# Optimization experiments

Measured on AMD Instinct MI355X. Metric: run time of the kernel, lower is better.

Reference implementation:

```python
import jax, jax.numpy as jnp
import numpy as np

INV_SQRT_2 = 0.5 ** 0.5

B, N, D_IN, D_OUT = 2, 50000, 64, 64
E = 800000


def setup_inputs() -> dict:
    key = jax.random.key(0)
    k1, k2, k3, k4, k5, k6 = jax.random.split(key, 6)
    x = jax.random.normal(k1, (B, N, D_IN, 3), dtype=jnp.float32)
    W_node = jax.random.normal(k2, (D_OUT, D_IN), dtype=jnp.float32)
    W_edge = jax.random.normal(k3, (D_OUT, D_IN), dtype=jnp.float32)
    norm_coeff = jax.random.uniform(k4, (N,), dtype=jnp.float32)
    src = jax.random.randint(k5, (E,), 0, N, dtype=jnp.int32)
    dst = jax.random.randint(k6, (E,), 0, N, dtype=jnp.int32)
    return {"x": x, "W_node": W_node, "W_edge": W_edge,
            "norm_coeff": norm_coeff, "src": src, "dst": dst}


def reference(x, W_node, W_edge, norm_coeff, src, dst):
    # x: (B, N, D_IN, 3)
    y_node = jnp.einsum('oi,bnik->bnok', W_node, x)      # (B, N, D_OUT, 3)
    y_edge = jnp.einsum('oi,bnik->bnok', W_edge, x)      # (B, N, D_OUT, 3)
    # gather by src along node axis, scatter-add into dst
    gathered = y_edge[:, src]                            # (B, E, D_OUT, 3)
    agg = jnp.zeros_like(y_node).at[:, dst].add(gathered)  # (B, N, D_OUT, 3)
    ans = y_node + norm_coeff[:, None, None] * agg
    return ans * INV_SQRT_2
```

## Files before the change

kernel.cpp:

```cpp
#include <hip/hip_runtime.h>
#include <hip/hip_bf16.h>

constexpr int B_   = 2;
constexpr int N_   = 50000;
constexpr int E_   = 800000;
constexpr int CAP  = 64;
constexpr int WPB  = 8;
constexpr float INV_SQRT_2 = 0.70710678118654752440f;

constexpr int SCAT_THREADS = E_ / 4;
constexpr int SCAT_BLKS    = (SCAT_THREADS + 255) / 256;
constexpr int CONV_ELEMS   = B_ * N_ * 192;
constexpr int CONV_THREADS = CONV_ELEMS / 8;
constexpr int CONV_BLKS    = CONV_THREADS / 256;


__global__ __launch_bounds__(256) void zero_kernel(int* __restrict__ p, int n) {
    int i = blockIdx.x * 256 + threadIdx.x;
    if (i < n) p[i] = 0;
}

__device__ __forceinline__ unsigned f2bf(float f) {
    unsigned u = __float_as_uint(f);
    return (u + 0x7fffu + ((u >> 16) & 1u)) >> 16;
}
__device__ __forceinline__ float blo(unsigned u) { return __uint_as_float(u << 16); }
__device__ __forceinline__ float bhi(unsigned u) { return __uint_as_float(u & 0xffff0000u); }

__global__ __launch_bounds__(256) void prep_kernel(
    const int* __restrict__ src,
    const int* __restrict__ dst,
    const float* __restrict__ x,
    int* counts,
    int* __restrict__ sorted_pad,
    unsigned* __restrict__ xbf)
{
    const int bid = blockIdx.x;
    if (bid < SCAT_BLKS) {
        int t = bid * 256 + threadIdx.x;
        if (t < SCAT_THREADS) {
            int4 dv = ((const int4*)dst)[t];
            int4 sv = ((const int4*)src)[t];
            int p0 = atomicAdd(&counts[dv.x], 1);
            int p1 = atomicAdd(&counts[dv.y], 1);
            int p2 = atomicAdd(&counts[dv.z], 1);
            int p3 = atomicAdd(&counts[dv.w], 1);
            if (p0 < CAP) sorted_pad[(dv.x << 6) + p0] = sv.x;
            if (p1 < CAP) sorted_pad[(dv.y << 6) + p1] = sv.y;
            if (p2 < CAP) sorted_pad[(dv.z << 6) + p2] = sv.z;
            if (p3 < CAP) sorted_pad[(dv.w << 6) + p3] = sv.w;
        }
    } else {
        int t = (bid - SCAT_BLKS) * 256 + threadIdx.x;
        const float4* xp = (const float4*)x;
        float4 a = xp[(size_t)t * 2 + 0];
        float4 c = xp[(size_t)t * 2 + 1];
        uint4 o;
        o.x = f2bf(a.x) | (f2bf(a.y) << 16);
        o.y = f2bf(a.z) | (f2bf(a.w) << 16);
        o.z = f2bf(c.x) | (f2bf(c.y) << 16);
        o.w = f2bf(c.z) | (f2bf(c.w) << 16);
        ((uint4*)xbf)[t] = o;
    }
}

__global__ __launch_bounds__(512, 8) void fused_kernel(
    const float* __restrict__ Wn,
    const float* __restrict__ We,
    const float* __restrict__ norm,
    const int* __restrict__ counts,
    const int* __restrict__ sorted_pad,
    const unsigned* __restrict__ xbf,
    float* __restrict__ out)
{
    __shared__ unsigned WnP[32][64];
    __shared__ unsigned WeP[32][64];
    __shared__ __align__(16) float xs[WPB][192];
    __shared__ __align__(16) float xa[WPB][192];

    for (int t = threadIdx.x; t < 2048; t += 512) {
        int i2 = t >> 6, o = t & 63;
        WnP[i2][o] = f2bf(Wn[o * 64 + 2 * i2]) | (f2bf(Wn[o * 64 + 2 * i2 + 1]) << 16);
        WeP[i2][o] = f2bf(We[o * 64 + 2 * i2]) | (f2bf(We[o * 64 + 2 * i2 + 1]) << 16);
    }
    __syncthreads();

    const int wave = threadIdx.x >> 6;
    const int lane = threadIdx.x & 63;
    const int p = blockIdx.x * WPB + wave;
    const int b = p / N_;
    const int d = p - b * N_;

    const int degc = counts[d];
    const int deg = degc < CAP ? degc : CAP;
    const int* sp = sorted_pad + (d << 6);
    const uint2* xb2 = (const uint2*)xbf + (size_t)b * N_ * 48;

    if (lane < 48) {
        uint2 ov = xb2[(size_t)d * 48 + lane];
        float4 s4;
        s4.x = blo(ov.x); s4.y = bhi(ov.x);
        s4.z = blo(ov.y); s4.w = bhi(ov.y);
        ((float4*)&xs[wave][0])[lane] = s4;

        float ax = 0.f, ay = 0.f, az = 0.f, aw = 0.f;
        int e = 0;
        for (; e + 7 < deg; e += 8) {
            int s0 = sp[e + 0], s1 = sp[e + 1], s2 = sp[e + 2], s3 = sp[e + 3];
            int s4i = sp[e + 4], s5 = sp[e + 5], s6 = sp[e + 6], s7 = sp[e + 7];
            uint2 v0 = xb2[(size_t)s0 * 48 + lane];
            uint2 v1 = xb2[(size_t)s1 * 48 + lane];
            uint2 v2 = xb2[(size_t)s2 * 48 + lane];
            uint2 v3 = xb2[(size_t)s3 * 48 + lane];
            uint2 v4 = xb2[(size_t)s4i * 48 + lane];
            uint2 v5 = xb2[(size_t)s5 * 48 + lane];
            uint2 v6 = xb2[(size_t)s6 * 48 + lane];
            uint2 v7 = xb2[(size_t)s7 * 48 + lane];
            ax += ((blo(v0.x) + blo(v1.x)) + (blo(v2.x) + blo(v3.x)))
                + ((blo(v4.x) + blo(v5.x)) + (blo(v6.x) + blo(v7.x)));
            ay += ((bhi(v0.x) + bhi(v1.x)) + (bhi(v2.x) + bhi(v3.x)))
                + ((bhi(v4.x) + bhi(v5.x)) + (bhi(v6.x) + bhi(v7.x)));
            az += ((blo(v0.y) + blo(v1.y)) + (blo(v2.y) + blo(v3.y)))
                + ((blo(v4.y) + blo(v5.y)) + (blo(v6.y) + blo(v7.y)));
            aw += ((bhi(v0.y) + bhi(v1.y)) + (bhi(v2.y) + bhi(v3.y)))
                + ((bhi(v4.y) + bhi(v5.y)) + (bhi(v6.y) + bhi(v7.y)));
        }
        for (; e < deg; ++e) {
            int s = sp[e];
            uint2 v = xb2[(size_t)s * 48 + lane];
            ax += blo(v.x); ay += bhi(v.x);
            az += blo(v.y); aw += bhi(v.y);
        }
        float4 a4; a4.x = ax; a4.y = ay; a4.z = az; a4.w = aw;
        ((float4*)&xa[wave][0])[lane] = a4;
    }

    float an0 = 0.f, an1 = 0.f, an2 = 0.f;
    float ae0 = 0.f, ae1 = 0.f, ae2 = 0.f;
    const float4* xsv = (const float4*)&xs[wave][0];
    const float4* xav = (const float4*)&xa[wave][0];

    #pragma unroll
    for (int i4 = 0; i4 < 16; ++i4) {
        unsigned un0 = WnP[2 * i4 + 0][lane];
        unsigned un1 = WnP[2 * i4 + 1][lane];
        unsigned ue0 = WeP[2 * i4 + 0][lane];
        unsigned ue1 = WeP[2 * i4 + 1][lane];
        float4 d0 = xsv[i4 * 3 + 0];
        float4 d1 = xsv[i4 * 3 + 1];
        float4 d2 = xsv[i4 * 3 + 2];
        float4 g0 = xav[i4 * 3 + 0];
        float4 g1 = xav[i4 * 3 + 1];
        float4 g2 = xav[i4 * 3 + 2];
        float wn0 = blo(un0), wn1 = bhi(un0), wn2 = blo(un1), wn3 = bhi(un1);
        float we0 = blo(ue0), we1 = bhi(ue0), we2 = blo(ue1), we3 = bhi(ue1);

        an0 = fmaf(wn0, d0.x, an0); an1 = fmaf(wn0, d0.y, an1); an2 = fmaf(wn0, d0.z, an2);
        an0 = fmaf(wn1, d0.w, an0); an1 = fmaf(wn1, d1.x, an1); an2 = fmaf(wn1, d1.y, an2);
        an0 = fmaf(wn2, d1.z, an0); an1 = fmaf(wn2, d1.w, an1); an2 = fmaf(wn2, d2.x, an2);
        an0 = fmaf(wn3, d2.y, an0); an1 = fmaf(wn3, d2.z, an1); an2 = fmaf(wn3, d2.w, an2);

        ae0 = fmaf(we0, g0.x, ae0); ae1 = fmaf(we0, g0.y, ae1); ae2 = fmaf(we0, g0.z, ae2);
        ae0 = fmaf(we1, g0.w, ae0); ae1 = fmaf(we1, g1.x, ae1); ae2 = fmaf(we1, g1.y, ae2);
        ae0 = fmaf(we2, g1.z, ae0); ae1 = fmaf(we2, g1.w, ae1); ae2 = fmaf(we2, g2.x, ae2);
        ae0 = fmaf(we3, g2.y, ae0); ae1 = fmaf(we3, g2.z, ae1); ae2 = fmaf(we3, g2.w, ae2);
    }

    const float sc = norm[d];
    const size_t off = (size_t)p * 192 + (size_t)lane * 3;
    out[off + 0] = INV_SQRT_2 * fmaf(sc, ae0, an0);
    out[off + 1] = INV_SQRT_2 * fmaf(sc, ae1, an1);
    out[off + 2] = INV_SQRT_2 * fmaf(sc, ae2, an2);
}

extern "C" void kernel_launch(void* const* d_in, const int* in_sizes, int n_in,
                              void* d_out, int out_size, void* d_ws, size_t ws_size,
                              hipStream_t stream) {
    const float* x    = (const float*)d_in[0];
    const float* Wn   = (const float*)d_in[1];
    const float* We   = (const float*)d_in[2];
    const float* norm = (const float*)d_in[3];
    const int*   src  = (const int*)d_in[4];
    const int*   dst  = (const int*)d_in[5];
    float* out = (float*)d_out;

    int* counts        = (int*)d_ws;
    int* sorted_pad    = counts + N_;
    unsigned* xbf      = (unsigned*)(sorted_pad + (size_t)CAP * N_);

    zero_kernel<<<(N_ + 255) / 256, 256, 0, stream>>>(counts, N_);
    prep_kernel<<<SCAT_BLKS + CONV_BLKS, 256, 0, stream>>>(src, dst, x, counts,
                                                           sorted_pad, xbf);
    fused_kernel<<<(B_ * N_) / WPB, 512, 0, stream>>>(Wn, We, norm, counts,
                                                      sorted_pad, xbf, out);
}
```

Before: 481.5 us.

## Replace atomic padded bucketing with two-level radix sort into CSR layout

Swaps the global-atomic per-destination padded slot list (capped at 64 neighbours) for a two-pass radix sort. It builds a per-block histogram over high destination bits, runs a multi-kernel prefix scan, scatters into bins, then sorts locally within each bin to produce CSR offsets and sorted sources. The aggregation kernel reads neighbours from contiguous CSR ranges, which removes the degree cap and the scattered global atomics. Output stores are now staged through shared memory so each wave writes coalesced float4s. The cost is several extra small kernel launches plus the mid-buffer traffic, and sources are packed into 16 bits, which relies on N fitting in 65536.

After: 449.0 us. -6.8%, faster.

```diff
diff --git a/kernel.cpp b/kernel.cpp
--- a/kernel.cpp
+++ b/kernel.cpp
@@ -4,21 +4,26 @@
 constexpr int B_   = 2;
 constexpr int N_   = 50000;
 constexpr int E_   = 800000;
-constexpr int CAP  = 64;
 constexpr int WPB  = 8;
 constexpr float INV_SQRT_2 = 0.70710678118654752440f;
 
-constexpr int SCAT_THREADS = E_ / 4;
-constexpr int SCAT_BLKS    = (SCAT_THREADS + 255) / 256;
-constexpr int CONV_ELEMS   = B_ * N_ * 192;
-constexpr int CONV_THREADS = CONV_ELEMS / 8;
+constexpr int NBIN = 256;
+constexpr int EPB  = 4096;
+constexpr int HBLK = (E_ + EPB - 1) / EPB;
+constexpr int MSZ  = NBIN * HBLK;
+constexpr int SBLK = (MSZ + 255) / 256;
+
+constexpr int CONV_THREADS = B_ * N_ * 192 / 8;
 constexpr int CONV_BLKS    = CONV_THREADS / 256;
 
-
-__global__ __launch_bounds__(256) void zero_kernel(int* __restrict__ p, int n) {
-    int i = blockIdx.x * 256 + threadIdx.x;
-    if (i < n) p[i] = 0;
-}
+constexpr int OFF_CNT  = 0;
+constexpr int OFF_SCAN = MSZ;
+constexpr int OFF_BSUM = 2 * MSZ;
+constexpr int OFF_BSX  = 2 * MSZ + SBLK;
+constexpr int OFF_MID  = 2 * MSZ + 2 * SBLK;
+constexpr int OFF_SORT = OFF_MID + E_;
+constexpr int OFF_OFFS = OFF_SORT + E_;
+constexpr int OFF_XBF  = ((OFF_OFFS + N_ + 1 + 3) / 4) * 4;
 
 __device__ __forceinline__ unsigned f2bf(float f) {
     unsigned u = __float_as_uint(f);
@@ -27,50 +32,150 @@
 __device__ __forceinline__ float blo(unsigned u) { return __uint_as_float(u << 16); }
 __device__ __forceinline__ float bhi(unsigned u) { return __uint_as_float(u & 0xffff0000u); }
 
-__global__ __launch_bounds__(256) void prep_kernel(
-    const int* __restrict__ src,
-    const int* __restrict__ dst,
-    const float* __restrict__ x,
-    int* counts,
-    int* __restrict__ sorted_pad,
-    unsigned* __restrict__ xbf)
+__global__ __launch_bounds__(256) void hist_conv_kernel(
+    const int* __restrict__ dst, const float* __restrict__ x,
+    int* __restrict__ cnt, unsigned* __restrict__ xbf)
 {
+    __shared__ int h[NBIN];
     const int bid = blockIdx.x;
-    if (bid < SCAT_BLKS) {
-        int t = bid * 256 + threadIdx.x;
-        if (t < SCAT_THREADS) {
-            int4 dv = ((const int4*)dst)[t];
-            int4 sv = ((const int4*)src)[t];
-            int p0 = atomicAdd(&counts[dv.x], 1);
-            int p1 = atomicAdd(&counts[dv.y], 1);
-            int p2 = atomicAdd(&counts[dv.z], 1);
-            int p3 = atomicAdd(&counts[dv.w], 1);
-            if (p0 < CAP) sorted_pad[(dv.x << 6) + p0] = sv.x;
-            if (p1 < CAP) sorted_pad[(dv.y << 6) + p1] = sv.y;
-            if (p2 < CAP) sorted_pad[(dv.z << 6) + p2] = sv.z;
-            if (p3 < CAP) sorted_pad[(dv.w << 6) + p3] = sv.w;
+    const int t = threadIdx.x;
+    if (bid < HBLK) {
+        h[t] = 0;
+        __syncthreads();
+        const int e0 = bid * EPB;
+        #pragma unroll
+        for (int it = 0; it < EPB / 256; ++it) {
+            int e = e0 + it * 256 + t;
+            if (e < E_) atomicAdd(&h[dst[e] >> 8], 1);
         }
+        __syncthreads();
+        cnt[t * HBLK + bid] = h[t];
     } else {
-        int t = (bid - SCAT_BLKS) * 256 + threadIdx.x;
+        int i = (bid - HBLK) * 256 + t;
         const float4* xp = (const float4*)x;
-        float4 a = xp[(size_t)t * 2 + 0];
-        float4 c = xp[(size_t)t * 2 + 1];
+        float4 a = xp[(size_t)i * 2 + 0];
+        float4 c = xp[(size_t)i * 2 + 1];
         uint4 o;
         o.x = f2bf(a.x) | (f2bf(a.y) << 16);
         o.y = f2bf(a.z) | (f2bf(a.w) << 16);
         o.z = f2bf(c.x) | (f2bf(c.y) << 16);
         o.w = f2bf(c.z) | (f2bf(c.w) << 16);
-        ((uint4*)xbf)[t] = o;
+        ((uint4*)xbf)[i] = o;
+    }
+}
+
+__global__ __launch_bounds__(256) void scan_partial_kernel(const int* __restrict__ cnt,
+                                                           int* __restrict__ bsum) {
+    __shared__ int w[4];
+    int idx = blockIdx.x * 256 + threadIdx.x;
+    int v = (idx < MSZ) ? cnt[idx] : 0;
+    #pragma unroll
+    for (int o = 32; o; o >>= 1) v += __shfl_down(v, o, 64);
+    if ((threadIdx.x & 63) == 0) w[threadIdx.x >> 6] = v;
+    __syncthreads();
+    if (threadIdx.x == 0) bsum[blockIdx.x] = w[0] + w[1] + w[2] + w[3];
+}
+
+__global__ __launch_bounds__(256) void scan_bsum_kernel(const int* __restrict__ bsum,
+                                                        int* __restrict__ bsx) {
+    __shared__ int tmp[256];
+    int t = threadIdx.x;
+    int v = (t < SBLK) ? bsum[t] : 0;
+    tmp[t] = v;
+    __syncthreads();
+    #pragma unroll
+    for (int off = 1; off < 256; off <<= 1) {
+        int u = (t >= off) ? tmp[t - off] : 0;
+        __syncthreads();
+        tmp[t] += u;
+        __syncthreads();
+    }
+    if (t < SBLK) bsx[t] = tmp[t] - v;
+}
+
+__global__ __launch_bounds__(256) void scan_final_kernel(const int* __restrict__ cnt,
+                                                         const int* __restrict__ bsx,
+                                                         int* __restrict__ scanned) {
+    __shared__ int tmp[256];
+    int idx = blockIdx.x * 256 + threadIdx.x;
+    int t = threadIdx.x;
+    int v = (idx < MSZ) ? cnt[idx] : 0;
+    tmp[t] = v;
+    __syncthreads();
+    #pragma unroll
+    for (int off = 1; off < 256; off <<= 1) {
+        int u = (t >= off) ? tmp[t - off] : 0;
+        __syncthreads();
+        tmp[t] += u;
+        __syncthreads();
+    }
+    if (idx < MSZ) scanned[idx] = bsx[blockIdx.x] + tmp[t] - v;
+}
+
+__global__ __launch_bounds__(256) void mid_scatter_kernel(
+    const int* __restrict__ src, const int* __restrict__ dst,
+    const int* __restrict__ scanned, unsigned* __restrict__ mid)
+{
+    __shared__ int lbase[NBIN];
+    __shared__ int lrank[NBIN];
+    const int t = threadIdx.x, blk = blockIdx.x;
+    lbase[t] = scanned[t * HBLK + blk];
+    lrank[t] = 0;
+    __syncthreads();
+    const int e0 = blk * EPB;
+    #pragma unroll
+    for (int it = 0; it < EPB / 256; ++it) {
+        int e = e0 + it * 256 + t;
+        if (e < E_) {
+            int d = dst[e];
+            int bin = d >> 8;
+            int r = atomicAdd(&lrank[bin], 1);
+            mid[lbase[bin] + r] = ((unsigned)d << 16) | (unsigned)src[e];
+        }
+    }
+}
+
+__global__ __launch_bounds__(256) void bucket_sort_kernel(
+    const unsigned* __restrict__ mid, const int* __restrict__ scanned,
+    int* __restrict__ sortedsrc, int* __restrict__ offsets)
+{
+    __shared__ int h[NBIN], pfx[NBIN], rank[NBIN];
+    const int t = threadIdx.x, b = blockIdx.x;
+    const int r0 = scanned[b * HBLK];
+    const int r1 = scanned[(b + 1) * HBLK];
+    h[t] = 0;
+    __syncthreads();
+    for (int e = r0 + t; e < r1; e += 256)
+        atomicAdd(&h[(mid[e] >> 16) & 255], 1);
+    __syncthreads();
+    int v = h[t];
+    pfx[t] = v;
+    __syncthreads();
+    #pragma unroll
+    for (int off = 1; off < 256; off <<= 1) {
+        int u = (t >= off) ? pfx[t - off] : 0;
+        __syncthreads();
+        pfx[t] += u;
+        __syncthreads();
+    }
+    pfx[t] -= v;
+    rank[t] = 0;
+    int d = (b << 8) + t;
+    if (d < N_) offsets[d] = r0 + pfx[t];
+    if (b == 0 && t == 0) offsets[N_] = E_;
+    __syncthreads();
+    for (int e = r0 + t; e < r1; e += 256) {
+        unsigned pk = mid[e];
+        int bin = (pk >> 16) & 255;
+        int slot = r0 + pfx[bin] + atomicAdd(&rank[bin], 1);
+        sortedsrc[slot] = (int)(pk & 0xFFFFu);
     }
 }
 
 __global__ __launch_bounds__(512, 8) void fused_kernel(
-    const float* __restrict__ Wn,
-    const float* __restrict__ We,
-    const float* __restrict__ norm,
-    const int* __restrict__ counts,
-    const int* __restrict__ sorted_pad,
-    const unsigned* __restrict__ xbf,
+    const float* __restrict__ Wn, const float* __restrict__ We,
+    const float* __restrict__ norm, const int* __restrict__ offsets,
+    const int* __restrict__ sortedsrc, const unsigned* __restrict__ xbf,
     float* __restrict__ out)
 {
     __shared__ unsigned WnP[32][64];
@@ -91,9 +196,10 @@
     const int b = p / N_;
     const int d = p - b * N_;
 
-    const int degc = counts[d];
-    const int deg = degc < CAP ? degc : CAP;
-    const int* sp = sorted_pad + (d << 6);
+    const int beg = offsets[d];
+    const int end = offsets[d + 1];
+    const int deg = end - beg;
+    const int* sp = sortedsrc + beg;
     const uint2* xb2 = (const uint2*)xbf + (size_t)b * N_ * 48;
 
     if (lane < 48) {
@@ -167,10 +273,14 @@
     }
 
     const float sc = norm[d];
-    const size_t off = (size_t)p * 192 + (size_t)lane * 3;
-    out[off + 0] = INV_SQRT_2 * fmaf(sc, ae0, an0);
-    out[off + 1] = INV_SQRT_2 * fmaf(sc, ae1, an1);
-    out[off + 2] = INV_SQRT_2 * fmaf(sc, ae2, an2);
+    float* xw = &xs[wave][0];
+    xw[lane * 3 + 0] = INV_SQRT_2 * fmaf(sc, ae0, an0);
+    xw[lane * 3 + 1] = INV_SQRT_2 * fmaf(sc, ae1, an1);
+    xw[lane * 3 + 2] = INV_SQRT_2 * fmaf(sc, ae2, an2);
+    if (lane < 48) {
+        float4 o4 = ((const float4*)xw)[lane];
+        ((float4*)(out + (size_t)p * 192))[lane] = o4;
+    }
 }
 
 extern "C" void kernel_launch(void* const* d_in, const int* in_sizes, int n_in,
@@ -184,13 +294,22 @@
     const int*   dst  = (const int*)d_in[5];
     float* out = (float*)d_out;
 
-    int* counts        = (int*)d_ws;
-    int* sorted_pad    = counts + N_;
-    unsigned* xbf      = (unsigned*)(sorted_pad + (size_t)CAP * N_);
-
-    zero_kernel<<<(N_ + 255) / 256, 256, 0, stream>>>(counts, N_);
-    prep_kernel<<<SCAT_BLKS + CONV_BLKS, 256, 0, stream>>>(src, dst, x, counts,
-                                                           sorted_pad, xbf);
-    fused_kernel<<<(B_ * N_) / WPB, 512, 0, stream>>>(Wn, We, norm, counts,
-                                                      sorted_pad, xbf, out);
-}
+    int* ws_i          = (int*)d_ws;
+    int* cnt           = ws_i + OFF_CNT;
+    int* scanned       = ws_i + OFF_SCAN;
+    int* bsum          = ws_i + OFF_BSUM;
+    int* bsx           = ws_i + OFF_BSX;
+    unsigned* mid      = (unsigned*)(ws_i + OFF_MID);
+    int* sortedsrc     = ws_i + OFF_SORT;
+    int* offsets       = ws_i + OFF_OFFS;
+    unsigned* xbf      = (unsigned*)(ws_i + OFF_XBF);
+
+    hist_conv_kernel<<<HBLK + CONV_BLKS, 256, 0, stream>>>(dst, x, cnt, xbf);
+    scan_partial_kernel<<<SBLK, 256, 0, stream>>>(cnt, bsum);
+    scan_bsum_kernel<<<1, 256, 0, stream>>>(bsum, bsx);
+    scan_final_kernel<<<SBLK, 256, 0, stream>>>(cnt, bsx, scanned);
+    mid_scatter_kernel<<<HBLK, 256, 0, stream>>>(src, dst, scanned, mid);
+    bucket_sort_kernel<<<HBLK, 256, 0, stream>>>(mid, scanned, sortedsrc, offsets);
+    fused_kernel<<<(B_ * N_) / WPB, 512, 0, stream>>>(Wn, We, norm, offsets,
+                                                      sortedsrc, xbf, out);
+}
```
